# Kernel tuning notes

Hardware: AMD Instinct MI355X
Metric: run time of the kernel (lower is better)

## Reference

```python
import jax, jax.numpy as jnp
import numpy as np

HIDDEN = 4096
NUM_HEADS = 32
HEAD_DIM = HIDDEN // NUM_HEADS


def _fp8_roundtrip(x):
    # emulate torch float8_e4m3fn weight storage
    return x.astype(jnp.float8_e4m3fn).astype(jnp.float32)


def setup_inputs() -> dict:
    key = jax.random.key(0)
    ks = jax.random.split(key, 10)
    B, S = 2, 4096
    hidden_states = jax.random.normal(ks[0], (B, S, HIDDEN), dtype=jnp.float32)
    scale = 0.02
    def lin(kw, kb):
        w = jax.random.normal(kw, (HIDDEN, HIDDEN), dtype=jnp.float32) * scale
        b = jax.random.normal(kb, (HIDDEN,), dtype=jnp.float32) * scale
        return w, b
    wq, bq = lin(ks[1], ks[2])
    wk, bk = lin(ks[3], ks[4])
    wv, bv = lin(ks[5], ks[6])
    wl, bl = lin(ks[7], ks[8])
    # fp8-quantized Q/K/V projections (latent projection stays fp32)
    wq, bq = _fp8_roundtrip(wq), _fp8_roundtrip(bq)
    wk, bk = _fp8_roundtrip(wk), _fp8_roundtrip(bk)
    wv, bv = _fp8_roundtrip(wv), _fp8_roundtrip(bv)
    return {"hidden_states": hidden_states, "wq": wq, "bq": bq, "wk": wk,
            "bk": bk, "wv": wv, "bv": bv, "wl": wl, "bl": bl}


def reference(hidden_states, wq, bq, wk, bk, wv, bv, wl, bl):
    B, S, E = hidden_states.shape
    H, D = NUM_HEADS, HEAD_DIM
    q = (hidden_states @ wq.T + bq).reshape(B, S, H, D)
    k = (hidden_states @ wk.T + bk).reshape(B, S, H, D)
    v = (hidden_states @ wv.T + bv).reshape(B, S, H, D)
    latent = hidden_states @ wl.T + bl  # computed but unused, as in source
    # NOTE: source does NOT transpose to [B,H,S,D]; scores are [B,S,H,H]
    scores = jnp.einsum('bshd,bstd->bsht', q, k) / np.sqrt(D).astype(np.float32)
    probs = jax.nn.softmax(scores, axis=-1)
    context = jnp.einsum('bsht,bstd->bshd', probs, v).reshape(B, S, E)
    return context
```

## Files before the change

kernel.cpp:

```cpp
#include <hip/hip_runtime.h>
#include <stdint.h>

#define HIDDEN 4096
#define M_TOK 8192
#define KDIM 4096

typedef __attribute__((ext_vector_type(8))) __bf16 bf16x8;
typedef __attribute__((ext_vector_type(4))) float f32x4;
typedef __attribute__((ext_vector_type(8))) unsigned short u16x8;

#define GAS __attribute__((address_space(1)))
#define LAS __attribute__((address_space(3)))

__device__ __forceinline__ unsigned short f2bf(float f) {
  unsigned int u = __float_as_uint(f);
  u += 0x7FFFu + ((u >> 16) & 1u);
  return (unsigned short)(u >> 16);
}
__device__ __forceinline__ float bf2f(unsigned short b) {
  return __uint_as_float(((unsigned int)b) << 16);
}

__global__ __launch_bounds__(256) void cvt_kernel(const float* __restrict__ in,
                                                  unsigned short* __restrict__ out,
                                                  int n8) {
  int i = blockIdx.x * 256 + threadIdx.x;
  if (i >= n8) return;
  const f32x4* p = (const f32x4*)in + (size_t)2 * i;
  f32x4 a = p[0], b = p[1];
  u16x8 o;
  o[0] = f2bf(a.x); o[1] = f2bf(a.y); o[2] = f2bf(a.z); o[3] = f2bf(a.w);
  o[4] = f2bf(b.x); o[5] = f2bf(b.y); o[6] = f2bf(b.z); o[7] = f2bf(b.w);
  ((u16x8*)out)[i] = o;
}

#define BAR() __builtin_amdgcn_s_barrier()
#define PRIO(p) __builtin_amdgcn_s_setprio(p)
#define VMC6() asm volatile("s_waitcnt vmcnt(6)" ::: "memory")
#define VMC4() asm volatile("s_waitcnt vmcnt(4)" ::: "memory")
#define VMC0() asm volatile("s_waitcnt vmcnt(0)" ::: "memory")
#define PH_MID() do { __builtin_amdgcn_s_barrier(); \
  asm volatile("s_waitcnt lgkmcnt(0)" ::: "memory"); \
  __builtin_amdgcn_sched_barrier(0); } while (0)

__global__ __launch_bounds__(512, 2) void gemm_qkv(
    const unsigned short* __restrict__ A,
    const unsigned short* __restrict__ W,
    const float* __restrict__ bias,
    unsigned short* __restrict__ out) {
  __shared__ __attribute__((aligned(16))) unsigned short lds[65536];

  int tid = threadIdx.x;
  int lane = tid & 63;
  int w = tid >> 6;
  int wm = w >> 2;
  int wn = w & 3;
  int l16 = lane & 15;
  int lk = lane >> 4;

  int bid = blockIdx.x;
  int xcd = bid & 7;
  int local = bid >> 3;
  int r = local >> 5;
  int i = local & 31;
  int tm = (xcd << 2) + (i >> 3);
  int tn = (r << 3) + (i & 7);
  int m0 = tm << 8, n0 = tn << 8;

  int rp = tid >> 3;
  int ce = ((tid & 7) << 3) ^ ((rp & 7) << 3);
  const unsigned short* aSrc = A + (size_t)(m0 + rp) * KDIM + ce;
  const unsigned short* bSrc = W + (size_t)(n0 + rp) * KDIM + ce;
  int tid8 = tid * 8;

#define STA(b, h, kt) do { \
  __builtin_amdgcn_global_load_lds((GAS void*)(aSrc + (size_t)((h)*128) * KDIM + (kt)*64), \
      (LAS void*)(lds + (b)*16384 + (h)*8192 + tid8), 16, 0, 0); \
  __builtin_amdgcn_global_load_lds((GAS void*)(aSrc + (size_t)((h)*128 + 64) * KDIM + (kt)*64), \
      (LAS void*)(lds + (b)*16384 + (h)*8192 + 4096 + tid8), 16, 0, 0); } while (0)
#define STB(b, h, kt) do { \
  __builtin_amdgcn_global_load_lds((GAS void*)(bSrc + (size_t)((h)*128) * KDIM + (kt)*64), \
      (LAS void*)(lds + 32768 + (b)*16384 + (h)*8192 + tid8), 16, 0, 0); \
  __builtin_amdgcn_global_load_lds((GAS void*)(bSrc + (size_t)((h)*128 + 64) * KDIM + (kt)*64), \
      (LAS void*)(lds + 32768 + (b)*16384 + (h)*8192 + 4096 + tid8), 16, 0, 0); } while (0)

  int colbase = (lk << 3) ^ ((l16 & 7) << 3);
  int aRd = wm * 8192 + l16 * 64 + colbase;
  int bRd = (wn >> 1) * 8192 + (wn & 1) * 4096 + l16 * 64 + colbase;

#define RD_A(c, mi, ks) (*(const bf16x8*)(lds + (c)*16384 + (((aRd) + (mi)*1024) ^ ((ks)*32))))
#define RD_B(c, nj, ks) (*(const bf16x8*)(lds + 32768 + (c)*16384 + (((bRd) + (nj)*1024) ^ ((ks)*32))))

  bf16x8 av[8][2];
  bf16x8 bv[4][2];
  f32x4 acc[8][4] = {};

#define RP1(c) do { \
  bv[0][0]=RD_B(c,0,0); bv[0][1]=RD_B(c,0,1); bv[1][0]=RD_B(c,1,0); bv[1][1]=RD_B(c,1,1); \
  bv[2][0]=RD_B(c,2,0); bv[2][1]=RD_B(c,2,1); bv[3][0]=RD_B(c,3,0); bv[3][1]=RD_B(c,3,1); \
  av[0][0]=RD_A(c,0,0); av[0][1]=RD_A(c,0,1); av[1][0]=RD_A(c,1,0); av[1][1]=RD_A(c,1,1); } while (0)
#define RP2(c) do { \
  av[2][0]=RD_A(c,2,0); av[2][1]=RD_A(c,2,1); av[3][0]=RD_A(c,3,0); av[3][1]=RD_A(c,3,1); \
  av[4][0]=RD_A(c,4,0); av[4][1]=RD_A(c,4,1); av[5][0]=RD_A(c,5,0); av[5][1]=RD_A(c,5,1); } while (0)
#define RP3(c) do { \
  av[6][0]=RD_A(c,6,0); av[6][1]=RD_A(c,6,1); av[7][0]=RD_A(c,7,0); av[7][1]=RD_A(c,7,1); } while (0)

#define MFMA2(mi, nj) do { \
  acc[mi][nj] = __builtin_amdgcn_mfma_f32_16x16x32_bf16(av[mi][0], bv[nj][0], acc[mi][nj], 0, 0, 0); \
  acc[mi][nj] = __builtin_amdgcn_mfma_f32_16x16x32_bf16(av[mi][1], bv[nj][1], acc[mi][nj], 0, 0, 0); } while (0)
#define MM(mi) do { MFMA2(mi,0); MFMA2(mi,1); MFMA2(mi,2); MFMA2(mi,3); } while (0)

  STB(0, 0, 0); STB(0, 1, 0); STA(0, 0, 0); STA(0, 1, 0);
  VMC4();
  STB(1, 0, 1); STB(1, 1, 1); STA(1, 0, 1);
  VMC6();
  BAR();

  for (int it = 0; it < 31; ++it) {
    int k1 = 2 * it + 1, k2 = 2 * it + 2, k3 = 2 * it + 3;
    RP1(0); STA(1, 1, k1); PH_MID(); PRIO(1); MM(0); MM(1); PRIO(0); BAR();
    RP2(0); STB(0, 0, k2); PH_MID(); PRIO(1); MM(2); MM(3); PRIO(0); BAR();
    RP3(0); STB(0, 1, k2); PH_MID(); PRIO(1); MM(4); MM(5); PRIO(0); BAR();
            STA(0, 0, k2); PH_MID(); PRIO(1); MM(6); MM(7); PRIO(0); VMC6(); BAR();
    RP1(1); STA(0, 1, k2); PH_MID(); PRIO(1); MM(0); MM(1); PRIO(0); BAR();
    RP2(1); STB(1, 0, k3); PH_MID(); PRIO(1); MM(2); MM(3); PRIO(0); BAR();
    RP3(1); STB(1, 1, k3); PH_MID(); PRIO(1); MM(4); MM(5); PRIO(0); BAR();
            STA(1, 0, k3); PH_MID(); PRIO(1); MM(6); MM(7); PRIO(0); VMC6(); BAR();
  }
  RP1(0); STA(1, 1, 63); PH_MID(); PRIO(1); MM(0); MM(1); PRIO(0); BAR();
  RP2(0);                PH_MID(); PRIO(1); MM(2); MM(3); PRIO(0); BAR();
  RP3(0);                PH_MID(); PRIO(1); MM(4); MM(5); PRIO(0); BAR();
                         PH_MID(); PRIO(1); MM(6); MM(7); PRIO(0); VMC0(); BAR();
  RP1(1);                PH_MID(); PRIO(1); MM(0); MM(1); PRIO(0); BAR();
  RP2(1);                PH_MID(); PRIO(1); MM(2); MM(3); PRIO(0); BAR();
  RP3(1);                PH_MID(); PRIO(1); MM(4); MM(5); PRIO(0); BAR();
                         PH_MID(); PRIO(1); MM(6); MM(7); PRIO(0);

  int matc = n0 >> 12;
  int ncol = (n0 & 4095) + wn * 64;
  unsigned short* O = out + (size_t)matc * M_TOK * HIDDEN;
  float bb[4];
#pragma unroll
  for (int nj = 0; nj < 4; ++nj) bb[nj] = bias[n0 + wn * 64 + nj * 16 + l16];
#pragma unroll
  for (int mi = 0; mi < 8; ++mi) {
#pragma unroll
    for (int r = 0; r < 4; ++r) {
      int row = m0 + wm * 128 + mi * 16 + lk * 4 + r;
      size_t rb = (size_t)row * HIDDEN + ncol + l16;
#pragma unroll
      for (int nj = 0; nj < 4; ++nj)
        O[rb + nj * 16] = f2bf(acc[mi][nj][r] + bb[nj]);
    }
  }
}

__global__ __launch_bounds__(256) void attn_kernel(const unsigned short* __restrict__ qkv,
                                                   float* __restrict__ out) {
  __shared__ float sQ[32 * 132];
  __shared__ float sK[32 * 132];
  __shared__ float sV[32 * 132];
  __shared__ float sP[32 * 33];

  int m = blockIdx.x;
  int tid = threadIdx.x;
  const unsigned short* gq = qkv + (size_t)m * HIDDEN;
  const unsigned short* gk = gq + (size_t)M_TOK * HIDDEN;
  const unsigned short* gv = gk + (size_t)M_TOK * HIDDEN;

  int row = tid >> 3;
  int cb = (tid & 7) << 4;
  int go = row * 128 + cb;
  int lo = row * 132 + cb;
  {
    u16x8 x0 = *(const u16x8*)(gq + go);
    u16x8 x1 = *(const u16x8*)(gq + go + 8);
#pragma unroll
    for (int j = 0; j < 8; ++j) { sQ[lo + j] = bf2f(x0[j]); sQ[lo + 8 + j] = bf2f(x1[j]); }
    x0 = *(const u16x8*)(gk + go);
    x1 = *(const u16x8*)(gk + go + 8);
#pragma unroll
    for (int j = 0; j < 8; ++j) { sK[lo + j] = bf2f(x0[j]); sK[lo + 8 + j] = bf2f(x1[j]); }
    x0 = *(const u16x8*)(gv + go);
    x1 = *(const u16x8*)(gv + go + 8);
#pragma unroll
    for (int j = 0; j < 8; ++j) { sV[lo + j] = bf2f(x0[j]); sV[lo + 8 + j] = bf2f(x1[j]); }
  }
  __syncthreads();

  int h = tid >> 3;
  int t4 = (tid & 7) << 2;
  const f32x4* qr = (const f32x4*)(sQ + h * 132);
  const f32x4* k0 = (const f32x4*)(sK + (t4 + 0) * 132);
  const f32x4* k1 = (const f32x4*)(sK + (t4 + 1) * 132);
  const f32x4* k2 = (const f32x4*)(sK + (t4 + 2) * 132);
  const f32x4* k3 = (const f32x4*)(sK + (t4 + 3) * 132);
  float s0 = 0.f, s1 = 0.f, s2 = 0.f, s3 = 0.f;
#pragma unroll
  for (int d = 0; d < 32; ++d) {
    f32x4 q = qr[d];
    f32x4 a = k0[d]; s0 += q.x * a.x + q.y * a.y + q.z * a.z + q.w * a.w;
    f32x4 b = k1[d]; s1 += q.x * b.x + q.y * b.y + q.z * b.z + q.w * b.w;
    f32x4 c = k2[d]; s2 += q.x * c.x + q.y * c.y + q.z * c.z + q.w * c.w;
    f32x4 e = k3[d]; s3 += q.x * e.x + q.y * e.y + q.z * e.z + q.w * e.w;
  }
  const float scale = 0.08838834764831845f;
  s0 *= scale; s1 *= scale; s2 *= scale; s3 *= scale;
  float mx = fmaxf(fmaxf(s0, s1), fmaxf(s2, s3));
  mx = fmaxf(mx, __shfl_xor(mx, 1));
  mx = fmaxf(mx, __shfl_xor(mx, 2));
  mx = fmaxf(mx, __shfl_xor(mx, 4));
  float e0 = __expf(s0 - mx), e1 = __expf(s1 - mx), e2 = __expf(s2 - mx), e3 = __expf(s3 - mx);
  float sum = e0 + e1 + e2 + e3;
  sum += __shfl_xor(sum, 1);
  sum += __shfl_xor(sum, 2);
  sum += __shfl_xor(sum, 4);
  float inv = 1.0f / sum;
  sP[h * 33 + t4 + 0] = e0 * inv;
  sP[h * 33 + t4 + 1] = e1 * inv;
  sP[h * 33 + t4 + 2] = e2 * inv;
  sP[h * 33 + t4 + 3] = e3 * inv;
  __syncthreads();

  int d0 = (tid & 7) << 4;
  f32x4 o0 = {0.f, 0.f, 0.f, 0.f}, o1 = o0, o2 = o0, o3 = o0;
  const float* pr = sP + h * 33;
#pragma unroll
  for (int t = 0; t < 32; ++t) {
    float p = pr[t];
    const f32x4* vr = (const f32x4*)(sV + t * 132 + d0);
    o0 += p * vr[0];
    o1 += p * vr[1];
    o2 += p * vr[2];
    o3 += p * vr[3];
  }
  f32x4* op = (f32x4*)(out + (size_t)m * HIDDEN + h * 128 + d0);
  op[0] = o0; op[1] = o1; op[2] = o2; op[3] = o3;
}

extern "C" void kernel_launch(void* const* d_in, const int* in_sizes, int n_in,
                              void* d_out, int out_size, void* d_ws, size_t ws_size,
                              hipStream_t stream) {
  const float* hs = (const float*)d_in[0];
  const float* wq = (const float*)d_in[1];
  const float* bq = (const float*)d_in[2];
  const float* wk = (const float*)d_in[3];
  const float* bk = (const float*)d_in[4];
  const float* wv = (const float*)d_in[5];
  const float* bv = (const float*)d_in[6];

  char* ws = (char*)d_ws;
  const size_t HS_OFF = 0;
  const size_t W_OFF = 67108864;
  const size_t QKV_OFF = 167772160;
  const size_t BIAS_OFF = 369098752;
  const size_t NEED = 369147904;
  if (ws_size < NEED) return;

  unsigned short* hsb = (unsigned short*)(ws + HS_OFF);
  unsigned short* wb = (unsigned short*)(ws + W_OFF);
  unsigned short* qkv = (unsigned short*)(ws + QKV_OFF);
  float* bias = (float*)(ws + BIAS_OFF);

  cvt_kernel<<<16384, 256, 0, stream>>>(hs, hsb, 4194304);
  cvt_kernel<<<8192, 256, 0, stream>>>(wq, wb, 2097152);
  cvt_kernel<<<8192, 256, 0, stream>>>(wk, wb + 16777216, 2097152);
  cvt_kernel<<<8192, 256, 0, stream>>>(wv, wb + 33554432, 2097152);
  hipMemcpyAsync(bias, bq, 16384, hipMemcpyDeviceToDevice, stream);
  hipMemcpyAsync(bias + 4096, bk, 16384, hipMemcpyDeviceToDevice, stream);
  hipMemcpyAsync(bias + 8192, bv, 16384, hipMemcpyDeviceToDevice, stream);

  gemm_qkv<<<1536, 512, 0, stream>>>(hsb, wb, bias, qkv);
  attn_kernel<<<8192, 256, 0, stream>>>(qkv, (float*)d_out);
}
```

Measured before the change: 865.2 us.

## Shrink QKV GEMM tile to 128x128 with simpler double-buffered pipeline

Replaces the 256x256 block tile with a 128x128 tile, quadrupling the grid. LDS use is halved and launch bounds are raised to allow four blocks per CU. The eight-phase interleaved schedule becomes a simple two-stage double buffer: each stage reads all fragments, issues the next loads, then runs all MFMAs. This trades lower arithmetic intensity, meaning more global and LDS traffic per FLOP, for higher occupancy and a simpler schedule.

```diff
diff --git a/kernel.cpp b/kernel.cpp
--- a/kernel.cpp
+++ b/kernel.cpp
@@ -36,19 +36,18 @@
 
 #define BAR() __builtin_amdgcn_s_barrier()
 #define PRIO(p) __builtin_amdgcn_s_setprio(p)
-#define VMC6() asm volatile("s_waitcnt vmcnt(6)" ::: "memory")
 #define VMC4() asm volatile("s_waitcnt vmcnt(4)" ::: "memory")
 #define VMC0() asm volatile("s_waitcnt vmcnt(0)" ::: "memory")
-#define PH_MID() do { __builtin_amdgcn_s_barrier(); \
-  asm volatile("s_waitcnt lgkmcnt(0)" ::: "memory"); \
+#define LGKM0() do { asm volatile("s_waitcnt lgkmcnt(0)" ::: "memory"); \
   __builtin_amdgcn_sched_barrier(0); } while (0)
-
-__global__ __launch_bounds__(512, 2) void gemm_qkv(
+#define SB0() __builtin_amdgcn_sched_barrier(0)
+
+__global__ __launch_bounds__(512, 4) void gemm_qkv(
     const unsigned short* __restrict__ A,
     const unsigned short* __restrict__ W,
     const float* __restrict__ bias,
     unsigned short* __restrict__ out) {
-  __shared__ __attribute__((aligned(16))) unsigned short lds[65536];
+  __shared__ __attribute__((aligned(16))) unsigned short lds[32768];
 
   int tid = threadIdx.x;
   int lane = tid & 63;
@@ -61,11 +60,11 @@
   int bid = blockIdx.x;
   int xcd = bid & 7;
   int local = bid >> 3;
-  int r = local >> 5;
-  int i = local & 31;
-  int tm = (xcd << 2) + (i >> 3);
+  int r = local >> 6;
+  int i = local & 63;
+  int tm = (xcd << 3) + (i >> 3);
   int tn = (r << 3) + (i & 7);
-  int m0 = tm << 8, n0 = tn << 8;
+  int m0 = tm << 7, n0 = tn << 7;
 
   int rp = tid >> 3;
   int ce = ((tid & 7) << 3) ^ ((rp & 7) << 3);
@@ -73,84 +72,73 @@
   const unsigned short* bSrc = W + (size_t)(n0 + rp) * KDIM + ce;
   int tid8 = tid * 8;
 
-#define STA(b, h, kt) do { \
-  __builtin_amdgcn_global_load_lds((GAS void*)(aSrc + (size_t)((h)*128) * KDIM + (kt)*64), \
-      (LAS void*)(lds + (b)*16384 + (h)*8192 + tid8), 16, 0, 0); \
-  __builtin_amdgcn_global_load_lds((GAS void*)(aSrc + (size_t)((h)*128 + 64) * KDIM + (kt)*64), \
-      (LAS void*)(lds + (b)*16384 + (h)*8192 + 4096 + tid8), 16, 0, 0); } while (0)
-#define STB(b, h, kt) do { \
-  __builtin_amdgcn_global_load_lds((GAS void*)(bSrc + (size_t)((h)*128) * KDIM + (kt)*64), \
-      (LAS void*)(lds + 32768 + (b)*16384 + (h)*8192 + tid8), 16, 0, 0); \
-  __builtin_amdgcn_global_load_lds((GAS void*)(bSrc + (size_t)((h)*128 + 64) * KDIM + (kt)*64), \
-      (LAS void*)(lds + 32768 + (b)*16384 + (h)*8192 + 4096 + tid8), 16, 0, 0); } while (0)
+#define STA(b, kt) do { \
+  __builtin_amdgcn_global_load_lds((GAS void*)(aSrc + (kt)*64), \
+      (LAS void*)(lds + (b)*8192 + tid8), 16, 0, 0); \
+  __builtin_amdgcn_global_load_lds((GAS void*)(aSrc + (size_t)64 * KDIM + (kt)*64), \
+      (LAS void*)(lds + (b)*8192 + 4096 + tid8), 16, 0, 0); } while (0)
+#define STB(b, kt) do { \
+  __builtin_amdgcn_global_load_lds((GAS void*)(bSrc + (kt)*64), \
+      (LAS void*)(lds + 16384 + (b)*8192 + tid8), 16, 0, 0); \
+  __builtin_amdgcn_global_load_lds((GAS void*)(bSrc + (size_t)64 * KDIM + (kt)*64), \
+      (LAS void*)(lds + 16384 + (b)*8192 + 4096 + tid8), 16, 0, 0); } while (0)
 
   int colbase = (lk << 3) ^ ((l16 & 7) << 3);
-  int aRd = wm * 8192 + l16 * 64 + colbase;
-  int bRd = (wn >> 1) * 8192 + (wn & 1) * 4096 + l16 * 64 + colbase;
-
-#define RD_A(c, mi, ks) (*(const bf16x8*)(lds + (c)*16384 + (((aRd) + (mi)*1024) ^ ((ks)*32))))
-#define RD_B(c, nj, ks) (*(const bf16x8*)(lds + 32768 + (c)*16384 + (((bRd) + (nj)*1024) ^ ((ks)*32))))
-
-  bf16x8 av[8][2];
-  bf16x8 bv[4][2];
-  f32x4 acc[8][4] = {};
-
-#define RP1(c) do { \
+  int aRd = wm * 4096 + l16 * 64 + colbase;
+  int bRd = wn * 2048 + l16 * 64 + colbase;
+
+#define RD_A(c, mi, ks) (*(const bf16x8*)(lds + (c)*8192 + (((aRd) + (mi)*1024) ^ ((ks)*32))))
+#define RD_B(c, nj, ks) (*(const bf16x8*)(lds + 16384 + (c)*8192 + (((bRd) + (nj)*1024) ^ ((ks)*32))))
+
+  bf16x8 av[4][2];
+  bf16x8 bv[2][2];
+  f32x4 acc[4][2] = {};
+
+#define READS(c) do { \
   bv[0][0]=RD_B(c,0,0); bv[0][1]=RD_B(c,0,1); bv[1][0]=RD_B(c,1,0); bv[1][1]=RD_B(c,1,1); \
-  bv[2][0]=RD_B(c,2,0); bv[2][1]=RD_B(c,2,1); bv[3][0]=RD_B(c,3,0); bv[3][1]=RD_B(c,3,1); \
-  av[0][0]=RD_A(c,0,0); av[0][1]=RD_A(c,0,1); av[1][0]=RD_A(c,1,0); av[1][1]=RD_A(c,1,1); } while (0)
-#define RP2(c) do { \
-  av[2][0]=RD_A(c,2,0); av[2][1]=RD_A(c,2,1); av[3][0]=RD_A(c,3,0); av[3][1]=RD_A(c,3,1); \
-  av[4][0]=RD_A(c,4,0); av[4][1]=RD_A(c,4,1); av[5][0]=RD_A(c,5,0); av[5][1]=RD_A(c,5,1); } while (0)
-#define RP3(c) do { \
-  av[6][0]=RD_A(c,6,0); av[6][1]=RD_A(c,6,1); av[7][0]=RD_A(c,7,0); av[7][1]=RD_A(c,7,1); } while (0)
-
-#define MFMA2(mi, nj) do { \
-  acc[mi][nj] = __builtin_amdgcn_mfma_f32_16x16x32_bf16(av[mi][0], bv[nj][0], acc[mi][nj], 0, 0, 0); \
-  acc[mi][nj] = __builtin_amdgcn_mfma_f32_16x16x32_bf16(av[mi][1], bv[nj][1], acc[mi][nj], 0, 0, 0); } while (0)
-#define MM(mi) do { MFMA2(mi,0); MFMA2(mi,1); MFMA2(mi,2); MFMA2(mi,3); } while (0)
-
-  STB(0, 0, 0); STB(0, 1, 0); STA(0, 0, 0); STA(0, 1, 0);
-  VMC4();
-  STB(1, 0, 1); STB(1, 1, 1); STA(1, 0, 1);
-  VMC6();
+  av[0][0]=RD_A(c,0,0); av[0][1]=RD_A(c,0,1); av[1][0]=RD_A(c,1,0); av[1][1]=RD_A(c,1,1); \
+  av[2][0]=RD_A(c,2,0); av[2][1]=RD_A(c,2,1); av[3][0]=RD_A(c,3,0); av[3][1]=RD_A(c,3,1); } while (0)
+
+#define MF(mi, nj, ks) acc[mi][nj] = __builtin_amdgcn_mfma_f32_16x16x32_bf16( \
+    av[mi][ks], bv[nj][ks], acc[mi][nj], 0, 0, 0)
+#define MFMAS() do { \
+  MF(0,0,0); MF(0,1,0); MF(1,0,0); MF(1,1,0); MF(2,0,0); MF(2,1,0); MF(3,0,0); MF(3,1,0); \
+  MF(0,0,1); MF(0,1,1); MF(1,0,1); MF(1,1,1); MF(2,0,1); MF(2,1,1); MF(3,0,1); MF(3,1,1); } while (0)
+
+  STA(0, 0); STB(0, 0); STA(1, 1); STB(1, 1);
+  VMC0();
   BAR();
 
   for (int it = 0; it < 31; ++it) {
-    int k1 = 2 * it + 1, k2 = 2 * it + 2, k3 = 2 * it + 3;
-    RP1(0); STA(1, 1, k1); PH_MID(); PRIO(1); MM(0); MM(1); PRIO(0); BAR();
-    RP2(0); STB(0, 0, k2); PH_MID(); PRIO(1); MM(2); MM(3); PRIO(0); BAR();
-    RP3(0); STB(0, 1, k2); PH_MID(); PRIO(1); MM(4); MM(5); PRIO(0); BAR();
-            STA(0, 0, k2); PH_MID(); PRIO(1); MM(6); MM(7); PRIO(0); VMC6(); BAR();
-    RP1(1); STA(0, 1, k2); PH_MID(); PRIO(1); MM(0); MM(1); PRIO(0); BAR();
-    RP2(1); STB(1, 0, k3); PH_MID(); PRIO(1); MM(2); MM(3); PRIO(0); BAR();
-    RP3(1); STB(1, 1, k3); PH_MID(); PRIO(1); MM(4); MM(5); PRIO(0); BAR();
-            STA(1, 0, k3); PH_MID(); PRIO(1); MM(6); MM(7); PRIO(0); VMC6(); BAR();
-  }
-  RP1(0); STA(1, 1, 63); PH_MID(); PRIO(1); MM(0); MM(1); PRIO(0); BAR();
-  RP2(0);                PH_MID(); PRIO(1); MM(2); MM(3); PRIO(0); BAR();
-  RP3(0);                PH_MID(); PRIO(1); MM(4); MM(5); PRIO(0); BAR();
-                         PH_MID(); PRIO(1); MM(6); MM(7); PRIO(0); VMC0(); BAR();
-  RP1(1);                PH_MID(); PRIO(1); MM(0); MM(1); PRIO(0); BAR();
-  RP2(1);                PH_MID(); PRIO(1); MM(2); MM(3); PRIO(0); BAR();
-  RP3(1);                PH_MID(); PRIO(1); MM(4); MM(5); PRIO(0); BAR();
-                         PH_MID(); PRIO(1); MM(6); MM(7); PRIO(0);
+    int k2 = 2 * it + 2, k3 = 2 * it + 3;
+    READS(0); LGKM0(); BAR();
+    STA(0, k2); STB(0, k2); SB0();
+    PRIO(1); MFMAS(); PRIO(0);
+    VMC4(); BAR();
+    READS(1); LGKM0(); BAR();
+    STA(1, k3); STB(1, k3); SB0();
+    PRIO(1); MFMAS(); PRIO(0);
+    VMC4(); BAR();
+  }
+  READS(0); LGKM0(); BAR();
+  PRIO(1); MFMAS(); PRIO(0);
+  VMC0(); BAR();
+  READS(1); LGKM0(); BAR();
+  PRIO(1); MFMAS(); PRIO(0);
 
   int matc = n0 >> 12;
-  int ncol = (n0 & 4095) + wn * 64;
+  int ncol = (n0 & 4095) + wn * 32;
   unsigned short* O = out + (size_t)matc * M_TOK * HIDDEN;
-  float bb[4];
-#pragma unroll
-  for (int nj = 0; nj < 4; ++nj) bb[nj] = bias[n0 + wn * 64 + nj * 16 + l16];
-#pragma unroll
-  for (int mi = 0; mi < 8; ++mi) {
-#pragma unroll
-    for (int r = 0; r < 4; ++r) {
-      int row = m0 + wm * 128 + mi * 16 + lk * 4 + r;
+  float bb0 = bias[n0 + wn * 32 + l16];
+  float bb1 = bias[n0 + wn * 32 + 16 + l16];
+#pragma unroll
+  for (int mi = 0; mi < 4; ++mi) {
+#pragma unroll
+    for (int rr = 0; rr < 4; ++rr) {
+      int row = m0 + wm * 64 + mi * 16 + lk * 4 + rr;
       size_t rb = (size_t)row * HIDDEN + ncol + l16;
-#pragma unroll
-      for (int nj = 0; nj < 4; ++nj)
-        O[rb + nj * 16] = f2bf(acc[mi][nj][r] + bb[nj]);
+      O[rb] = f2bf(acc[mi][0][rr] + bb0);
+      O[rb + 16] = f2bf(acc[mi][1][rr] + bb1);
     }
   }
 }
@@ -270,6 +258,6 @@
   hipMemcpyAsync(bias + 4096, bk, 16384, hipMemcpyDeviceToDevice, stream);
   hipMemcpyAsync(bias + 8192, bv, 16384, hipMemcpyDeviceToDevice, stream);
 
-  gemm_qkv<<<1536, 512, 0, stream>>>(hsb, wb, bias, qkv);
+  gemm_qkv<<<6144, 512, 0, stream>>>(hsb, wb, bias, qkv);
   attn_kernel<<<8192, 256, 0, stream>>>(qkv, (float*)d_out);
 }
```

After: 977.9 us. 1.13x slower.

## Fuse conversion launches and restructure GEMM LDS-read/MFMA phase scheduling

Applied to the files above, without the earlier changes.

Replaces four conversion kernels and three bias memcpys with one fused kernel that dispatches on block index. This removes launch and memcpy overheads. The GEMM main loop is also reorganized: LDS fragment reads are issued earlier, and partial lgkmcnt waits replace the full wait after each barrier, so MFMAs can start while the remaining LDS reads are still in flight. This raises register pressure and depends on the lgkmcnt counts matching the number of outstanding reads.

```diff
diff --git a/kernel.cpp b/kernel.cpp
--- a/kernel.cpp
+++ b/kernel.cpp
@@ -21,11 +21,8 @@
   return __uint_as_float(((unsigned int)b) << 16);
 }
 
-__global__ __launch_bounds__(256) void cvt_kernel(const float* __restrict__ in,
-                                                  unsigned short* __restrict__ out,
-                                                  int n8) {
-  int i = blockIdx.x * 256 + threadIdx.x;
-  if (i >= n8) return;
+__device__ __forceinline__ void cvt8(const float* __restrict__ in,
+                                     unsigned short* __restrict__ out, int i) {
   const f32x4* p = (const f32x4*)in + (size_t)2 * i;
   f32x4 a = p[0], b = p[1];
   u16x8 o;
@@ -34,14 +31,38 @@
   ((u16x8*)out)[i] = o;
 }
 
+__global__ __launch_bounds__(256) void cvt_fused(
+    const float* __restrict__ hs, const float* __restrict__ wq,
+    const float* __restrict__ wk, const float* __restrict__ wv,
+    const float* __restrict__ bq, const float* __restrict__ bk,
+    const float* __restrict__ bv,
+    unsigned short* __restrict__ hsb, unsigned short* __restrict__ wb,
+    float* __restrict__ bias) {
+  int b = blockIdx.x;
+  int tid = threadIdx.x;
+  if (b < 16384) {
+    cvt8(hs, hsb, b * 256 + tid);
+  } else if (b < 24576) {
+    cvt8(wq, wb, (b - 16384) * 256 + tid);
+  } else if (b < 32768) {
+    cvt8(wk, wb + 16777216, (b - 24576) * 256 + tid);
+  } else if (b < 40960) {
+    cvt8(wv, wb + 33554432, (b - 32768) * 256 + tid);
+  } else {
+    int i = (b - 40960) * 256 + tid;
+    float v = (i < 4096) ? bq[i] : (i < 8192) ? bk[i - 4096] : bv[i - 8192];
+    bias[i] = v;
+  }
+}
+
 #define BAR() __builtin_amdgcn_s_barrier()
 #define PRIO(p) __builtin_amdgcn_s_setprio(p)
 #define VMC6() asm volatile("s_waitcnt vmcnt(6)" ::: "memory")
 #define VMC4() asm volatile("s_waitcnt vmcnt(4)" ::: "memory")
 #define VMC0() asm volatile("s_waitcnt vmcnt(0)" ::: "memory")
-#define PH_MID() do { __builtin_amdgcn_s_barrier(); \
-  asm volatile("s_waitcnt lgkmcnt(0)" ::: "memory"); \
+#define LGKM(n) do { asm volatile("s_waitcnt lgkmcnt(" #n ")" ::: "memory"); \
   __builtin_amdgcn_sched_barrier(0); } while (0)
+#define SB0() __builtin_amdgcn_sched_barrier(0)
 
 __global__ __launch_bounds__(512, 2) void gemm_qkv(
     const unsigned short* __restrict__ A,
@@ -110,6 +131,16 @@
   acc[mi][nj] = __builtin_amdgcn_mfma_f32_16x16x32_bf16(av[mi][1], bv[nj][1], acc[mi][nj], 0, 0, 0); } while (0)
 #define MM(mi) do { MFMA2(mi,0); MFMA2(mi,1); MFMA2(mi,2); MFMA2(mi,3); } while (0)
 
+#define KTILE(c, ka, kb) do { \
+  RP1(c); RP2(c); STA(!(c), 1, ka); \
+  BAR(); LGKM(8); PRIO(1); MM(0); MM(1); PRIO(0); BAR(); \
+  RP3(c); STB(c, 0, kb); \
+  BAR(); LGKM(4); PRIO(1); MM(2); MM(3); PRIO(0); BAR(); \
+  STB(c, 1, kb); \
+  BAR(); LGKM(0); PRIO(1); MM(4); MM(5); PRIO(0); BAR(); \
+  STA(c, 0, kb); \
+  BAR(); SB0(); PRIO(1); MM(6); MM(7); PRIO(0); VMC6(); BAR(); } while (0)
+
   STB(0, 0, 0); STB(0, 1, 0); STA(0, 0, 0); STA(0, 1, 0);
   VMC4();
   STB(1, 0, 1); STB(1, 1, 1); STA(1, 0, 1);
@@ -118,23 +149,21 @@
 
   for (int it = 0; it < 31; ++it) {
     int k1 = 2 * it + 1, k2 = 2 * it + 2, k3 = 2 * it + 3;
-    RP1(0); STA(1, 1, k1); PH_MID(); PRIO(1); MM(0); MM(1); PRIO(0); BAR();
-    RP2(0); STB(0, 0, k2); PH_MID(); PRIO(1); MM(2); MM(3); PRIO(0); BAR();
-    RP3(0); STB(0, 1, k2); PH_MID(); PRIO(1); MM(4); MM(5); PRIO(0); BAR();
-            STA(0, 0, k2); PH_MID(); PRIO(1); MM(6); MM(7); PRIO(0); VMC6(); BAR();
-    RP1(1); STA(0, 1, k2); PH_MID(); PRIO(1); MM(0); MM(1); PRIO(0); BAR();
-    RP2(1); STB(1, 0, k3); PH_MID(); PRIO(1); MM(2); MM(3); PRIO(0); BAR();
-    RP3(1); STB(1, 1, k3); PH_MID(); PRIO(1); MM(4); MM(5); PRIO(0); BAR();
-            STA(1, 0, k3); PH_MID(); PRIO(1); MM(6); MM(7); PRIO(0); VMC6(); BAR();
-  }
-  RP1(0); STA(1, 1, 63); PH_MID(); PRIO(1); MM(0); MM(1); PRIO(0); BAR();
-  RP2(0);                PH_MID(); PRIO(1); MM(2); MM(3); PRIO(0); BAR();
-  RP3(0);                PH_MID(); PRIO(1); MM(4); MM(5); PRIO(0); BAR();
-                         PH_MID(); PRIO(1); MM(6); MM(7); PRIO(0); VMC0(); BAR();
-  RP1(1);                PH_MID(); PRIO(1); MM(0); MM(1); PRIO(0); BAR();
-  RP2(1);                PH_MID(); PRIO(1); MM(2); MM(3); PRIO(0); BAR();
-  RP3(1);                PH_MID(); PRIO(1); MM(4); MM(5); PRIO(0); BAR();
-                         PH_MID(); PRIO(1); MM(6); MM(7); PRIO(0);
+    KTILE(0, k1, k2);
+    KTILE(1, k2, k3);
+  }
+  RP1(0); RP2(0); STA(1, 1, 63);
+  BAR(); LGKM(8); PRIO(1); MM(0); MM(1); PRIO(0); BAR();
+  RP3(0);
+  BAR(); LGKM(4); PRIO(1); MM(2); MM(3); PRIO(0); BAR();
+  BAR(); LGKM(0); PRIO(1); MM(4); MM(5); PRIO(0); BAR();
+  BAR(); SB0(); PRIO(1); MM(6); MM(7); PRIO(0); VMC0(); BAR();
+  RP1(1); RP2(1);
+  BAR(); LGKM(8); PRIO(1); MM(0); MM(1); PRIO(0); BAR();
+  RP3(1);
+  BAR(); LGKM(4); PRIO(1); MM(2); MM(3); PRIO(0); BAR();
+  BAR(); LGKM(0); PRIO(1); MM(4); MM(5); PRIO(0); BAR();
+  BAR(); SB0(); PRIO(1); MM(6); MM(7); PRIO(0);
 
   int matc = n0 >> 12;
   int ncol = (n0 & 4095) + wn * 64;
@@ -145,12 +174,12 @@
 #pragma unroll
   for (int mi = 0; mi < 8; ++mi) {
 #pragma unroll
-    for (int r = 0; r < 4; ++r) {
-      int row = m0 + wm * 128 + mi * 16 + lk * 4 + r;
+    for (int rr = 0; rr < 4; ++rr) {
+      int row = m0 + wm * 128 + mi * 16 + lk * 4 + rr;
       size_t rb = (size_t)row * HIDDEN + ncol + l16;
 #pragma unroll
       for (int nj = 0; nj < 4; ++nj)
-        O[rb + nj * 16] = f2bf(acc[mi][nj][r] + bb[nj]);
+        O[rb + nj * 16] = f2bf(acc[mi][nj][rr] + bb[nj]);
     }
   }
 }
@@ -262,14 +291,7 @@
   unsigned short* qkv = (unsigned short*)(ws + QKV_OFF);
   float* bias = (float*)(ws + BIAS_OFF);
 
-  cvt_kernel<<<16384, 256, 0, stream>>>(hs, hsb, 4194304);
-  cvt_kernel<<<8192, 256, 0, stream>>>(wq, wb, 2097152);
-  cvt_kernel<<<8192, 256, 0, stream>>>(wk, wb + 16777216, 2097152);
-  cvt_kernel<<<8192, 256, 0, stream>>>(wv, wb + 33554432, 2097152);
-  hipMemcpyAsync(bias, bq, 16384, hipMemcpyDeviceToDevice, stream);
-  hipMemcpyAsync(bias + 4096, bk, 16384, hipMemcpyDeviceToDevice, stream);
-  hipMemcpyAsync(bias + 8192, bv, 16384, hipMemcpyDeviceToDevice, stream);
-
+  cvt_fused<<<41008, 256, 0, stream>>>(hs, wq, wk, wv, bq, bk, bv, hsb, wb, bias);
   gemm_qkv<<<1536, 512, 0, stream>>>(hsb, wb, bias, qkv);
   attn_kernel<<<8192, 256, 0, stream>>>(qkv, (float*)d_out);
 }
```

After: 865.0 us. Within noise of the previous version (-0.0%).
